# Performance work log

Hardware: AMD Instinct MI355X
Metric: run time of the kernel (lower is better)

The kernel has to match this reference:

```python
import jax, jax.numpy as jnp
import numpy as np

D_MODEL = 512
NUM_HEADS = 8
D_K = D_MODEL // NUM_HEADS


def setup_inputs() -> dict:
    key = jax.random.key(0)
    k0, k1, k2, k3, k4 = jax.random.split(key, 5)
    s = 1.0 / np.sqrt(D_MODEL)
    return {
        "x": jax.random.normal(k0, (2, 4096, D_MODEL), dtype=jnp.float32),
        "W_q": jax.random.normal(k1, (D_MODEL, D_MODEL), dtype=jnp.float32) * s,
        "W_k": jax.random.normal(k2, (D_MODEL, D_MODEL), dtype=jnp.float32) * s,
        "W_v": jax.random.normal(k3, (D_MODEL, D_MODEL), dtype=jnp.float32) * s,
        "W_o": jax.random.normal(k4, (D_MODEL, D_MODEL), dtype=jnp.float32) * s,
    }


def reference(x, W_q, W_k, W_v, W_o):
    B, S, _ = x.shape
    # project and split heads: (B, H, S, d_k)
    def split(t):
        return t.reshape(B, S, NUM_HEADS, D_K).transpose(0, 2, 1, 3)
    Q = split(x @ W_q)
    K = split(x @ W_k)
    V = split(x @ W_v)
    scale = jnp.sqrt(jnp.asarray(D_K, dtype=x.dtype))
    logits = jnp.einsum('bhqd,bhkd->bhqk', Q, K) / scale
    attn = jax.nn.softmax(logits, axis=-1)  # dropout is identity at inference
    out = jnp.einsum('bhqk,bhkd->bhqd', attn, V)
    concat = out.transpose(0, 2, 1, 3).reshape(B, S, D_MODEL)
    return concat @ W_o
```

## Files before the change

kernel.cpp:

```cpp
#include <hip/hip_runtime.h>
#include <hip/hip_bf16.h>


#define DMODEL 512
#define SEQ    4096
#define NTOK   8192
#define LDQK   1024

using f32x4 = __attribute__((ext_vector_type(4))) float;
using s16x8 = __attribute__((ext_vector_type(8))) short;
using u16x8 = __attribute__((ext_vector_type(8))) unsigned short;

static __device__ __forceinline__ unsigned short f2bf(float f) {
  union { float f; unsigned u; } v; v.f = f;
  unsigned r = v.u + 0x7fff + ((v.u >> 16) & 1);
  return (unsigned short)(r >> 16);
}

__global__ void cast_x_kernel(const float* __restrict__ x,
                              unsigned short* __restrict__ xb, int n4) {
  int i = blockIdx.x * blockDim.x + threadIdx.x;
  if (i >= n4) return;
  float4 v = ((const float4*)x)[i];
  ushort4 o;
  o.x = f2bf(v.x); o.y = f2bf(v.y); o.z = f2bf(v.z); o.w = f2bf(v.w);
  ((ushort4*)xb)[i] = o;
}

__global__ void wtrans4_kernel(const float* __restrict__ Wq,
                               const float* __restrict__ Wk,
                               const float* __restrict__ Wv,
                               const float* __restrict__ Wo,
                               unsigned short* __restrict__ Wall, float c2) {
  int y = blockIdx.y;
  int idx = blockIdx.x * 256 + threadIdx.x;
  const float* W = (y == 0) ? Wq : (y == 1) ? Wk : (y == 2) ? Wv : Wo;
  float scale = (y == 0) ? c2 : 1.0f;
  int k = idx & 511, n = idx >> 9;
  Wall[y * 262144 + idx] = f2bf(W[k * 512 + n] * scale);
}

__global__ __launch_bounds__(256, 3) void gemm_qkv(
    const unsigned short* __restrict__ xb,
    const unsigned short* __restrict__ Wall,
    unsigned short* __restrict__ QKb,
    unsigned short* __restrict__ Vtb)
{
  __shared__ unsigned short As[128 * 32];
  __shared__ unsigned short Bs[128 * 32];
  const int by = blockIdx.y;
  const bool vmode = (by >= 8);
  const unsigned short* A  = vmode ? (Wall + 2 * 262144) : xb;
  const unsigned short* Bt = vmode ? xb : Wall;
  const size_t bm = vmode ? (size_t)(by - 8) * 128 : (size_t)blockIdx.x * 128;
  const size_t bn = vmode ? (size_t)blockIdx.x * 128 : (size_t)by * 128;
  const int tid  = threadIdx.x;
  const int wave = tid >> 6, lane = tid & 63;
  const int q4 = lane >> 4, ln = lane & 15;
  const int wm = (wave >> 1) * 64, wn = (wave & 1) * 64;
  f32x4 acc[4][4] = {};
  const int srow = wave * 16 + (lane >> 2);
  const int scol = (lane & 3) * 8;

  u16x8 a0 = *(const u16x8*)(A  + (bm + srow)      * 512 + scol);
  u16x8 a1 = *(const u16x8*)(A  + (bm + 64 + srow) * 512 + scol);
  u16x8 b0 = *(const u16x8*)(Bt + (bn + srow)      * 512 + scol);
  u16x8 b1 = *(const u16x8*)(Bt + (bn + 64 + srow) * 512 + scol);

  for (int kt = 0; kt < 512; kt += 32) {
    __syncthreads();
    *(u16x8*)(As + srow * 32 + scol)        = a0;
    *(u16x8*)(As + (64 + srow) * 32 + scol) = a1;
    *(u16x8*)(Bs + srow * 32 + scol)        = b0;
    *(u16x8*)(Bs + (64 + srow) * 32 + scol) = b1;
    __syncthreads();
    if (kt + 32 < 512) {
      a0 = *(const u16x8*)(A  + (bm + srow)      * 512 + kt + 32 + scol);
      a1 = *(const u16x8*)(A  + (bm + 64 + srow) * 512 + kt + 32 + scol);
      b0 = *(const u16x8*)(Bt + (bn + srow)      * 512 + kt + 32 + scol);
      b1 = *(const u16x8*)(Bt + (bn + 64 + srow) * 512 + kt + 32 + scol);
    }
    s16x8 af[4], bfr[4];
#pragma unroll
    for (int i = 0; i < 4; i++)
      af[i] = *(const s16x8*)(As + (wm + i * 16 + ln) * 32 + q4 * 8);
#pragma unroll
    for (int i = 0; i < 4; i++)
      bfr[i] = *(const s16x8*)(Bs + (wn + i * 16 + ln) * 32 + q4 * 8);
#pragma unroll
    for (int mi = 0; mi < 4; mi++)
#pragma unroll
      for (int ni = 0; ni < 4; ni++)
        acc[mi][ni] = __builtin_amdgcn_mfma_f32_16x16x32_bf16(
            af[mi], bfr[ni], acc[mi][ni], 0, 0, 0);
  }
#pragma unroll
  for (int mi = 0; mi < 4; mi++)
#pragma unroll
    for (int r = 0; r < 4; ++r) {
      size_t row = bm + wm + mi * 16 + q4 * 4 + r;
#pragma unroll
      for (int ni = 0; ni < 4; ni++) {
        size_t col = bn + wn + ni * 16 + ln;
        unsigned short hv = f2bf(acc[mi][ni][r]);
        if (!vmode) {
          QKb[row * 1024 + col] = hv;
        } else {
          int b = (int)(col >> 12), s = (int)(col & 4095);
          int sp = (s & ~63) | ((s & 15) << 2) | ((s >> 4) & 3);
          Vtb[(size_t)b * 2097152 + row * 4096 + sp] = hv;
        }
      }
    }
}

__global__ __launch_bounds__(256, 2) void attn_kernel(
    const unsigned short* __restrict__ QK,
    const unsigned short* __restrict__ Vt,
    unsigned short* __restrict__ Oc)
{
  const int qt = blockIdx.x, h = blockIdx.y, b = blockIdx.z;
  const int tid = threadIdx.x, wave = tid >> 6, lane = tid & 63;
  const int q4 = lane >> 4, ln = lane & 15;
  __shared__ unsigned short Ks[64 * 72];
  __shared__ unsigned short Vs[64 * 72];
  __shared__ unsigned short Ps[4][32 * 72];
  const size_t rowbase = (size_t)b * SEQ;
  const size_t qrow0   = (size_t)qt * 128 + wave * 32;
  const unsigned short* Kp  = QK + rowbase * LDQK + 512 + h * 64;
  const unsigned short* VTp = Vt + ((size_t)(b * 8 + h) * 64) * SEQ;

  s16x8 qf[2][2];
#pragma unroll
  for (int mf = 0; mf < 2; ++mf) {
    const unsigned short* q = QK + (rowbase + qrow0 + mf * 16 + ln) * LDQK + h * 64;
    qf[mf][0] = *(const s16x8*)(q + q4 * 8);
    qf[mf][1] = *(const s16x8*)(q + 32 + q4 * 8);
  }
  f32x4 o[2][4] = {};
  float lp[2][4] = {};

  const int srow = tid >> 2;
  const int scol = (tid & 3) * 16;

  const unsigned short* kgp = Kp  + (size_t)srow * LDQK + scol;
  const unsigned short* vgp = VTp + (size_t)srow * SEQ  + scol;
  u16x8 kr  = *(const u16x8*)kgp;
  u16x8 kr2 = *(const u16x8*)(kgp + 8);
  u16x8 vr  = *(const u16x8*)vgp;
  u16x8 vr2 = *(const u16x8*)(vgp + 8);

  for (int t = 0; t < SEQ / 64; ++t) {
    __syncthreads();
    *(u16x8*)(Ks + srow * 72 + scol)     = kr;
    *(u16x8*)(Ks + srow * 72 + scol + 8) = kr2;
    *(u16x8*)(Vs + srow * 72 + scol)     = vr;
    *(u16x8*)(Vs + srow * 72 + scol + 8) = vr2;
    __syncthreads();
    if (t + 1 < SEQ / 64) {
      kgp += (size_t)64 * LDQK;
      vgp += 64;
      kr  = *(const u16x8*)kgp;
      kr2 = *(const u16x8*)(kgp + 8);
      vr  = *(const u16x8*)vgp;
      vr2 = *(const u16x8*)(vgp + 8);
    }
    f32x4 s4[2][4] = {};
#pragma unroll
    for (int ni = 0; ni < 4; ni++) {
      const unsigned short* kb = Ks + (ni * 16 + ln) * 72 + q4 * 8;
      s16x8 kf0 = *(const s16x8*)kb;
      s16x8 kf1 = *(const s16x8*)(kb + 32);
#pragma unroll
      for (int mf = 0; mf < 2; ++mf) {
        s4[mf][ni] = __builtin_amdgcn_mfma_f32_16x16x32_bf16(qf[mf][0], kf0, s4[mf][ni], 0, 0, 0);
        s4[mf][ni] = __builtin_amdgcn_mfma_f32_16x16x32_bf16(qf[mf][1], kf1, s4[mf][ni], 0, 0, 0);
      }
    }
    unsigned short* Pw = Ps[wave];
#pragma unroll
    for (int mf = 0; mf < 2; ++mf)
#pragma unroll
      for (int r = 0; r < 4; ++r) {
        float p0 = __builtin_amdgcn_exp2f(s4[mf][0][r]);
        float p1 = __builtin_amdgcn_exp2f(s4[mf][1][r]);
        float p2 = __builtin_amdgcn_exp2f(s4[mf][2][r]);
        float p3 = __builtin_amdgcn_exp2f(s4[mf][3][r]);
        lp[mf][r] += (p0 + p1) + (p2 + p3);
        __hip_bfloat162 lo = __float22bfloat162_rn(make_float2(p0, p1));
        __hip_bfloat162 hi = __float22bfloat162_rn(make_float2(p2, p3));
        uint2 w;
        w.x = *(unsigned*)&lo;
        w.y = *(unsigned*)&hi;
        *(uint2*)(Pw + (mf * 16 + q4 * 4 + r) * 72 + ln * 4) = w;
      }
#pragma unroll
    for (int ks = 0; ks < 2; ++ks) {
      s16x8 pf[2];
#pragma unroll
      for (int mf = 0; mf < 2; ++mf)
        pf[mf] = *(const s16x8*)(Pw + (mf * 16 + ln) * 72 + ks * 32 + q4 * 8);
#pragma unroll
      for (int ni = 0; ni < 4; ni++) {
        s16x8 vf = *(const s16x8*)(Vs + (ni * 16 + ln) * 72 + ks * 32 + q4 * 8);
#pragma unroll
        for (int mf = 0; mf < 2; ++mf)
          o[mf][ni] = __builtin_amdgcn_mfma_f32_16x16x32_bf16(pf[mf], vf, o[mf][ni], 0, 0, 0);
      }
    }
  }
#pragma unroll
  for (int mf = 0; mf < 2; ++mf)
#pragma unroll
    for (int r = 0; r < 4; ++r) {
      float l = lp[mf][r];
#pragma unroll
      for (int off = 1; off < 16; off <<= 1)
        l += __shfl_xor(l, off, 64);
      float inv = 1.0f / l;
      size_t row = rowbase + qrow0 + mf * 16 + q4 * 4 + r;
#pragma unroll
      for (int ni = 0; ni < 4; ni++)
        Oc[row * DMODEL + h * 64 + ni * 16 + ln] = f2bf(o[mf][ni][r] * inv);
    }
}

__global__ __launch_bounds__(256, 3) void gemm_out(
    const unsigned short* __restrict__ A,
    const unsigned short* __restrict__ Bt,
    float* __restrict__ C)
{
  __shared__ unsigned short As[128 * 32];
  __shared__ unsigned short Bs[64 * 32];
  const int tid  = threadIdx.x;
  const int wave = tid >> 6, lane = tid & 63;
  const int q4 = lane >> 4, ln = lane & 15;
  const size_t bm = (size_t)blockIdx.x * 128;
  const size_t bn = (size_t)blockIdx.y * 64;
  const int wm = (wave >> 1) * 64, wn = (wave & 1) * 32;
  f32x4 acc[4][2] = {};
  const int srow = wave * 16 + (lane >> 2);
  const int scol = (lane & 3) * 8;

  u16x8 a0 = *(const u16x8*)(A  + (bm + srow)      * 512 + scol);
  u16x8 a1 = *(const u16x8*)(A  + (bm + 64 + srow) * 512 + scol);
  u16x8 b0 = *(const u16x8*)(Bt + (bn + srow)      * 512 + scol);

  for (int kt = 0; kt < 512; kt += 32) {
    __syncthreads();
    *(u16x8*)(As + srow * 32 + scol)        = a0;
    *(u16x8*)(As + (64 + srow) * 32 + scol) = a1;
    *(u16x8*)(Bs + srow * 32 + scol)        = b0;
    __syncthreads();
    if (kt + 32 < 512) {
      a0 = *(const u16x8*)(A  + (bm + srow)      * 512 + kt + 32 + scol);
      a1 = *(const u16x8*)(A  + (bm + 64 + srow) * 512 + kt + 32 + scol);
      b0 = *(const u16x8*)(Bt + (bn + srow)      * 512 + kt + 32 + scol);
    }
    s16x8 af[4], bfr[2];
#pragma unroll
    for (int i = 0; i < 4; i++)
      af[i] = *(const s16x8*)(As + (wm + i * 16 + ln) * 32 + q4 * 8);
#pragma unroll
    for (int i = 0; i < 2; i++)
      bfr[i] = *(const s16x8*)(Bs + (wn + i * 16 + ln) * 32 + q4 * 8);
#pragma unroll
    for (int mi = 0; mi < 4; mi++)
#pragma unroll
      for (int ni = 0; ni < 2; ni++)
        acc[mi][ni] = __builtin_amdgcn_mfma_f32_16x16x32_bf16(
            af[mi], bfr[ni], acc[mi][ni], 0, 0, 0);
  }
#pragma unroll
  for (int mi = 0; mi < 4; mi++)
#pragma unroll
    for (int r = 0; r < 4; ++r) {
      size_t row = bm + wm + mi * 16 + q4 * 4 + r;
#pragma unroll
      for (int ni = 0; ni < 2; ni++)
        C[row * 512 + bn + wn + ni * 16 + ln] = acc[mi][ni][r];
    }
}

extern "C" void kernel_launch(void* const* d_in, const int* in_sizes, int n_in,
                              void* d_out, int out_size, void* d_ws, size_t ws_size,
                              hipStream_t stream) {
  const float* x  = (const float*)d_in[0];
  const float* Wq = (const float*)d_in[1];
  const float* Wk = (const float*)d_in[2];
  const float* Wv = (const float*)d_in[3];
  const float* Wo = (const float*)d_in[4];

  char* ws = (char*)d_ws;
  unsigned short* xb   = (unsigned short*)(ws);
  unsigned short* Wall = (unsigned short*)(ws + 8388608);
  unsigned short* QKb  = (unsigned short*)(ws + 10485760);
  unsigned short* Vtb  = (unsigned short*)(ws + 27262976);
  unsigned short* Oc   = (unsigned short*)(ws + 35651584);

  const float C2 = 0.125f * 1.44269504088896f;

  hipLaunchKernelGGL(cast_x_kernel, dim3(NTOK * DMODEL / 4 / 256), dim3(256), 0,
                     stream, x, xb, NTOK * DMODEL / 4);
  hipLaunchKernelGGL(wtrans4_kernel, dim3(1024, 4), dim3(256), 0, stream,
                     Wq, Wk, Wv, Wo, Wall, C2);
  hipLaunchKernelGGL(gemm_qkv, dim3(64, 12), dim3(256), 0, stream,
                     xb, Wall, QKb, Vtb);
  hipLaunchKernelGGL(attn_kernel, dim3(32, 8, 2), dim3(256), 0, stream,
                     QKb, Vtb, Oc);
  hipLaunchKernelGGL(gemm_out, dim3(64, 8), dim3(256), 0, stream,
                     Oc, Wall + 3 * 262144, (float*)d_out);
}
```

Measured before the change: 204.8 us.

## Keep softmax probabilities in registers by computing S transposed and permuting V

Swaps the MFMA operands so the score tile comes out transposed, with each lane holding consecutive key positions for one query row. The exponentiated probabilities can then be packed directly into bf16 MFMA A-fragments, with no round trip through the per-wave LDS P buffer. The V layout permutation in the projection kernel changes to match the new key ordering. Row sums now reduce across lane groups, and the per-row sum is fetched with a shuffle at the end. This removes an LDS store/load round trip and frees shared memory, which could allow higher occupancy.

```diff
diff --git a/kernel.cpp b/kernel.cpp
--- a/kernel.cpp
+++ b/kernel.cpp
@@ -15,6 +15,11 @@
   union { float f; unsigned u; } v; v.f = f;
   unsigned r = v.u + 0x7fff + ((v.u >> 16) & 1);
   return (unsigned short)(r >> 16);
+}
+
+static __device__ __forceinline__ unsigned pack_bf2(float lo, float hi) {
+  __hip_bfloat162 t = __float22bfloat162_rn(make_float2(lo, hi));
+  union { __hip_bfloat162 b; unsigned u; } c; c.b = t; return c.u;
 }
 
 __global__ void cast_x_kernel(const float* __restrict__ x,
@@ -107,7 +112,8 @@
           QKb[row * 1024 + col] = hv;
         } else {
           int b = (int)(col >> 12), s = (int)(col & 4095);
-          int sp = (s & ~63) | ((s & 15) << 2) | ((s >> 4) & 3);
+          int sp = (s & ~63) | (s & 32) | (((s >> 2) & 3) << 3) |
+                   (((s >> 4) & 1) << 2) | (s & 3);
           Vtb[(size_t)b * 2097152 + row * 4096 + sp] = hv;
         }
       }
@@ -124,7 +130,6 @@
   const int q4 = lane >> 4, ln = lane & 15;
   __shared__ unsigned short Ks[64 * 72];
   __shared__ unsigned short Vs[64 * 72];
-  __shared__ unsigned short Ps[4][32 * 72];
   const size_t rowbase = (size_t)b * SEQ;
   const size_t qrow0   = (size_t)qt * 128 + wave * 32;
   const unsigned short* Kp  = QK + rowbase * LDQK + 512 + h * 64;
@@ -138,7 +143,7 @@
     qf[mf][1] = *(const s16x8*)(q + 32 + q4 * 8);
   }
   f32x4 o[2][4] = {};
-  float lp[2][4] = {};
+  float lp[2] = {};
 
   const int srow = tid >> 2;
   const int scol = (tid & 3) * 16;
@@ -173,51 +178,56 @@
       s16x8 kf1 = *(const s16x8*)(kb + 32);
 #pragma unroll
       for (int mf = 0; mf < 2; ++mf) {
-        s4[mf][ni] = __builtin_amdgcn_mfma_f32_16x16x32_bf16(qf[mf][0], kf0, s4[mf][ni], 0, 0, 0);
-        s4[mf][ni] = __builtin_amdgcn_mfma_f32_16x16x32_bf16(qf[mf][1], kf1, s4[mf][ni], 0, 0, 0);
+        s4[mf][ni] = __builtin_amdgcn_mfma_f32_16x16x32_bf16(kf0, qf[mf][0], s4[mf][ni], 0, 0, 0);
+        s4[mf][ni] = __builtin_amdgcn_mfma_f32_16x16x32_bf16(kf1, qf[mf][1], s4[mf][ni], 0, 0, 0);
       }
     }
-    unsigned short* Pw = Ps[wave];
-#pragma unroll
-    for (int mf = 0; mf < 2; ++mf)
-#pragma unroll
-      for (int r = 0; r < 4; ++r) {
-        float p0 = __builtin_amdgcn_exp2f(s4[mf][0][r]);
-        float p1 = __builtin_amdgcn_exp2f(s4[mf][1][r]);
-        float p2 = __builtin_amdgcn_exp2f(s4[mf][2][r]);
-        float p3 = __builtin_amdgcn_exp2f(s4[mf][3][r]);
-        lp[mf][r] += (p0 + p1) + (p2 + p3);
-        __hip_bfloat162 lo = __float22bfloat162_rn(make_float2(p0, p1));
-        __hip_bfloat162 hi = __float22bfloat162_rn(make_float2(p2, p3));
-        uint2 w;
-        w.x = *(unsigned*)&lo;
-        w.y = *(unsigned*)&hi;
-        *(uint2*)(Pw + (mf * 16 + q4 * 4 + r) * 72 + ln * 4) = w;
+    s16x8 pf[2][2];
+#pragma unroll
+    for (int mf = 0; mf < 2; ++mf) {
+      float e[4][4];
+      float ls = 0.f;
+#pragma unroll
+      for (int ni = 0; ni < 4; ni++)
+#pragma unroll
+        for (int r = 0; r < 4; ++r) {
+          e[ni][r] = __builtin_amdgcn_exp2f(s4[mf][ni][r]);
+          ls += e[ni][r];
+        }
+      lp[mf] += ls;
+#pragma unroll
+      for (int ks = 0; ks < 2; ++ks) {
+        union { s16x8 v; unsigned u[4]; } pu;
+        pu.u[0] = pack_bf2(e[2 * ks][0],     e[2 * ks][1]);
+        pu.u[1] = pack_bf2(e[2 * ks][2],     e[2 * ks][3]);
+        pu.u[2] = pack_bf2(e[2 * ks + 1][0], e[2 * ks + 1][1]);
+        pu.u[3] = pack_bf2(e[2 * ks + 1][2], e[2 * ks + 1][3]);
+        pf[mf][ks] = pu.v;
       }
-#pragma unroll
-    for (int ks = 0; ks < 2; ++ks) {
-      s16x8 pf[2];
-#pragma unroll
-      for (int mf = 0; mf < 2; ++mf)
-        pf[mf] = *(const s16x8*)(Pw + (mf * 16 + ln) * 72 + ks * 32 + q4 * 8);
+    }
+#pragma unroll
+    for (int ks = 0; ks < 2; ++ks)
 #pragma unroll
       for (int ni = 0; ni < 4; ni++) {
         s16x8 vf = *(const s16x8*)(Vs + (ni * 16 + ln) * 72 + ks * 32 + q4 * 8);
 #pragma unroll
         for (int mf = 0; mf < 2; ++mf)
-          o[mf][ni] = __builtin_amdgcn_mfma_f32_16x16x32_bf16(pf[mf], vf, o[mf][ni], 0, 0, 0);
+          o[mf][ni] = __builtin_amdgcn_mfma_f32_16x16x32_bf16(pf[mf][ks], vf, o[mf][ni], 0, 0, 0);
       }
-    }
+  }
+#pragma unroll
+  for (int mf = 0; mf < 2; ++mf) {
+    float l = lp[mf];
+    l += __shfl_xor(l, 16, 64);
+    l += __shfl_xor(l, 32, 64);
+    lp[mf] = l;
   }
 #pragma unroll
   for (int mf = 0; mf < 2; ++mf)
 #pragma unroll
     for (int r = 0; r < 4; ++r) {
-      float l = lp[mf][r];
-#pragma unroll
-      for (int off = 1; off < 16; off <<= 1)
-        l += __shfl_xor(l, off, 64);
-      float inv = 1.0f / l;
+      float lv = __shfl(lp[mf], q4 * 4 + r, 64);
+      float inv = 1.0f / lv;
       size_t row = rowbase + qrow0 + mf * 16 + q4 * 4 + r;
 #pragma unroll
       for (int ni = 0; ni < 4; ni++)
```

Result: no change. 206.4 us (+0.8%).
